# Performance work log

Measured on AMD Instinct MI355X. Metric: run time of the kernel, lower is better.

Reference implementation:

```python
import jax, jax.numpy as jnp
import numpy as np

D_MODEL = 1024
HEADS = 16
D_K = D_MODEL // HEADS
D_FF = 4096
B, S = 4, 2048
EPS = 1e-5


def _layer_norm(x, gamma, beta):
    mu = jnp.mean(x, axis=-1, keepdims=True)
    var = jnp.mean(jnp.square(x - mu), axis=-1, keepdims=True)
    return (x - mu) * jax.lax.rsqrt(var + EPS) * gamma + beta


def setup_inputs() -> dict:
    key = jax.random.key(0)
    ks = jax.random.split(key, 16)
    s_in = 1.0 / np.sqrt(D_MODEL)
    s_ff = 1.0 / np.sqrt(D_FF)
    inp = {
        "x": jax.random.normal(ks[0], (B, S, D_MODEL), dtype=jnp.float32),
        "src_mask": jnp.ones((B, 1, 1, S), dtype=jnp.int32),
        "Wq": jax.random.uniform(ks[1], (D_MODEL, D_MODEL), jnp.float32, -s_in, s_in),
        "bq": jnp.zeros((D_MODEL,), jnp.float32),
        "Wk": jax.random.uniform(ks[2], (D_MODEL, D_MODEL), jnp.float32, -s_in, s_in),
        "bk": jnp.zeros((D_MODEL,), jnp.float32),
        "Wv": jax.random.uniform(ks[3], (D_MODEL, D_MODEL), jnp.float32, -s_in, s_in),
        "bv": jnp.zeros((D_MODEL,), jnp.float32),
        "Wo": jax.random.uniform(ks[4], (D_MODEL, D_MODEL), jnp.float32, -s_in, s_in),
        "bo": jnp.zeros((D_MODEL,), jnp.float32),
        "W1": jax.random.uniform(ks[5], (D_MODEL, D_FF), jnp.float32, -s_in, s_in),
        "b1": jnp.zeros((D_FF,), jnp.float32),
        "W2": jax.random.uniform(ks[6], (D_FF, D_MODEL), jnp.float32, -s_ff, s_ff),
        "b2": jnp.zeros((D_MODEL,), jnp.float32),
        "g1": jnp.ones((D_MODEL,), jnp.float32),
        "be1": jnp.zeros((D_MODEL,), jnp.float32),
        "g2": jnp.ones((D_MODEL,), jnp.float32),
        "be2": jnp.zeros((D_MODEL,), jnp.float32),
    }
    return inp


def reference(x, src_mask, Wq, bq, Wk, bk, Wv, bv, Wo, bo, W1, b1, W2, b2, g1, be1, g2, be2):
    Bn, L, _ = x.shape
    # Self-attention (dropout=0 / eval)
    q = (x @ Wq + bq).reshape(Bn, L, HEADS, D_K).transpose(0, 2, 1, 3)  # [B,H,L,dk]
    k = (x @ Wk + bk).reshape(Bn, L, HEADS, D_K).transpose(0, 2, 1, 3)
    v = (x @ Wv + bv).reshape(Bn, L, HEADS, D_K).transpose(0, 2, 1, 3)
    scores = jnp.einsum("bhqd,bhkd->bhqk", q, k) / np.sqrt(D_K).astype(np.float32)
    scores = jnp.where(src_mask == 0, -jnp.inf, scores)
    attn = jax.nn.softmax(scores, axis=-1)
    out = jnp.einsum("bhqk,bhkd->bhqd", attn, v)
    out = out.transpose(0, 2, 1, 3).reshape(Bn, L, D_MODEL)
    attn_out = out @ Wo + bo
    x = _layer_norm(x + attn_out, g1, be1)
    # FFN
    ffn = jax.nn.relu(x @ W1 + b1) @ W2 + b2
    x = _layer_norm(x + ffn, g2, be2)
    return x
```

## Files before the change

kernel.cpp:

```cpp
#include <hip/hip_runtime.h>
#include <hip/hip_bf16.h>
#include <cstdint>
#include <cstddef>

typedef __bf16 bf16;
typedef __bf16 bf16x8 __attribute__((ext_vector_type(8)));
typedef float  f32x4  __attribute__((ext_vector_type(4)));
typedef unsigned short u16x4 __attribute__((ext_vector_type(4)));
typedef uint32_t u32x4 __attribute__((ext_vector_type(4)));

static constexpr int D_MODEL = 1024;
static constexpr int HEADS   = 16;
static constexpr int D_KH    = 64;
static constexpr int D_FF    = 4096;
static constexpr int BATCH   = 4;
static constexpr int SEQ     = 2048;
static constexpr int MROWS   = BATCH * SEQ;

#define VMCNT(n) asm volatile("s_waitcnt vmcnt(" #n ")" ::: "memory")
#define LGKM0()                                            \
  do {                                                     \
    asm volatile("s_waitcnt lgkmcnt(0)" ::: "memory");     \
    __builtin_amdgcn_sched_barrier(0);                     \
  } while (0)

__device__ __forceinline__ unsigned short bfbits(float f) {
  return __builtin_bit_cast(unsigned short, (bf16)f);
}

__device__ __forceinline__ void gload_lds16(const void* g, void* l) {
  __builtin_amdgcn_global_load_lds(
      (__attribute__((address_space(1))) uint32_t*)(uintptr_t)g,
      (__attribute__((address_space(3))) uint32_t*)(uintptr_t)l, 16, 0, 0);
}

__global__ void k_cast_bf16(const float* __restrict__ in, bf16* __restrict__ out) {
  int i = (blockIdx.x * 256 + threadIdx.x) * 8;
  const float4* p = (const float4*)(in + i);
  float4 a = p[0], b = p[1];
  bf16x8 v;
  v[0] = (bf16)a.x; v[1] = (bf16)a.y; v[2] = (bf16)a.z; v[3] = (bf16)a.w;
  v[4] = (bf16)b.x; v[5] = (bf16)b.y; v[6] = (bf16)b.z; v[7] = (bf16)b.w;
  *(bf16x8*)(out + i) = v;
}

__global__ void k_mask_flags(const int* __restrict__ mask, uint32_t* __restrict__ flags) {
  __shared__ uint32_t sb[4];
  int tid = threadIdx.x;
  if (tid < 4) sb[tid] = 0;
  __syncthreads();
  int b = tid >> 5, t = tid & 31;
  const int4* p = (const int4*)(mask + b * SEQ + t * 64);
  int all = 1;
#pragma unroll
  for (int i = 0; i < 16; ++i) {
    int4 v = p[i];
    all &= v.x & v.y & v.z & v.w;
  }
  if (all) atomicOr(&sb[b], 1u << t);
  __syncthreads();
  if (tid < 4) flags[tid] = sb[tid];
}

struct TP4 { const float* src[4]; bf16* dst[4]; };
__global__ void k_transpose_cast4(TP4 p) {
  __shared__ float tile[64][65];
  const float* W = p.src[blockIdx.z];
  bf16* Wt = p.dst[blockIdx.z];
  int k0 = blockIdx.x * 64, n0 = blockIdx.y * 64;
  int c = threadIdx.x & 63, r0 = threadIdx.x >> 6;
#pragma unroll
  for (int i = 0; i < 16; ++i) {
    int r = r0 + i * 4;
    tile[r][c] = W[(size_t)(k0 + r) * 1024 + n0 + c];
  }
  __syncthreads();
#pragma unroll
  for (int i = 0; i < 16; ++i) {
    int r = r0 + i * 4;
    Wt[(size_t)(n0 + r) * 1024 + k0 + c] = (bf16)tile[c][r];
  }
}

__global__ void k_transpose_cast(const float* __restrict__ W, bf16* __restrict__ Wt,
                                 int K, int N) {
  __shared__ float tile[64][65];
  int k0 = blockIdx.x * 64, n0 = blockIdx.y * 64;
  int c = threadIdx.x & 63, r0 = threadIdx.x >> 6;
#pragma unroll
  for (int i = 0; i < 16; ++i) {
    int r = r0 + i * 4;
    tile[r][c] = W[(size_t)(k0 + r) * N + n0 + c];
  }
  __syncthreads();
#pragma unroll
  for (int i = 0; i < 16; ++i) {
    int r = r0 + i * 4;
    Wt[(size_t)(n0 + r) * K + k0 + c] = (bf16)tile[c][r];
  }
}

enum { EP_RELU = 0, EP_F32 = 1, EP_QKV = 2 };

template <int EPI, int NREP>
__global__ __launch_bounds__(512, 2) void k_gemm8(
    const bf16* __restrict__ A, const bf16* __restrict__ Bt,
    const float* __restrict__ bias, const float* __restrict__ bias2,
    const float* __restrict__ bias3,
    void* __restrict__ Cout, void* __restrict__ C2, void* __restrict__ C3,
    int N, int K) {
  extern __shared__ char smem[];
  constexpr int BN = NREP * 64;
  constexpr int HB = NREP / 2;
  const int tid = threadIdx.x;
  const int lane = tid & 63;
  const int wid = tid >> 6;
  const int wm = wid >> 2, wn = wid & 3;
  const int l15 = lane & 15, l4 = lane >> 4;
  const int bx = blockIdx.x, by = blockIdx.y;
  const int NI = K >> 7;

  const int c0 = tid, c1 = tid + 512;
  const bf16* baseA0 = A + (size_t)(bx * 256 + (c0 >> 3)) * K + ((c0 & 7) ^ ((c0 >> 3) & 7)) * 8;
  const bf16* baseA1 = A + (size_t)(bx * 256 + (c1 >> 3)) * K + ((c1 & 7) ^ ((c1 >> 3) & 7)) * 8;
  const bf16* baseB0 = Bt + (size_t)(by * BN + (c0 >> 3)) * K + ((c0 & 7) ^ ((c0 >> 3) & 7)) * 8;
  const bf16* baseB1 = Bt + (size_t)(by * BN + (c1 >> 3)) * K + ((c1 & 7) ^ ((c1 >> 3) & 7)) * 8;
  const size_t rowK128 = (size_t)128 * K;

  auto stA = [&](int h, int t, int buf) {
    gload_lds16(baseA0 + h * rowK128 + t * 64, smem + buf * 32768 + h * 16384 + c0 * 16);
    gload_lds16(baseA1 + h * rowK128 + t * 64, smem + buf * 32768 + h * 16384 + c1 * 16);
  };
  auto stB = [&](int h, int t, int buf) {
    gload_lds16(baseB0 + h * rowK128 + t * 64,
                smem + 65536 + buf * (HB * 16384) + h * 16384 + c0 * 16);
    gload_lds16(baseB1 + h * rowK128 + t * 64,
                smem + 65536 + buf * (HB * 16384) + h * 16384 + c1 * 16);
  };

  const int ch0 = (l4 ^ (l15 & 7)) * 16;
  const int ch1 = ((4 + l4) ^ (l15 & 7)) * 16;
  const int aoff = l15 * 128;
  int boffh[NREP];
#pragma unroll
  for (int n = 0; n < NREP; ++n) {
    int rB = wn * (NREP * 16) + n * 16 + l15;
    boffh[n] = (rB >> 7) * 16384 + (rB & 127) * 128;
  }

  f32x4 acc[8][NREP] = {};
  bf16x8 breg[NREP][2];

  stA(0, 0, 0); stA(1, 0, 0); stB(0, 0, 0);
  if constexpr (HB == 2) stB(1, 0, 0);
  stA(0, 1, 1); stA(1, 1, 1); stB(0, 1, 1);
  if constexpr (HB == 2) stB(1, 1, 1);

  for (int i = 0; i < NI; ++i) {
    const int t1 = 2 * i + 1, t2 = 2 * i + 2;
    const bool notfirst = (i > 0), notlast = (i + 1 < NI);
#pragma unroll
    for (int p = 0; p < 8; ++p) {
      const int q = p & 3;
      const char* Ab = smem + (p >> 2) * 32768 + wm * 16384;
      const char* Bb = smem + 65536 + (p >> 2) * (HB * 16384);
      if (p == 0) {
        if (notfirst) {
          stA(0, t1, 1);
          VMCNT(2);
        } else {
          if constexpr (HB == 2) VMCNT(8); else VMCNT(6);
        }
        __builtin_amdgcn_s_barrier();
      } else if (p == 4) {
        if (notlast) {
          stA(0, t2, 0);
          VMCNT(2);
        } else {
          VMCNT(0);
        }
        __builtin_amdgcn_s_barrier();
      }
      if (q == 0) {
#pragma unroll
        for (int n = 0; n < NREP; ++n) {
          breg[n][0] = *(const bf16x8*)(Bb + boffh[n] + ch0);
          breg[n][1] = *(const bf16x8*)(Bb + boffh[n] + ch1);
        }
      }
      bf16x8 a0k0 = *(const bf16x8*)(Ab + (2 * q + 0) * 2048 + aoff + ch0);
      bf16x8 a0k1 = *(const bf16x8*)(Ab + (2 * q + 0) * 2048 + aoff + ch1);
      bf16x8 a1k0 = *(const bf16x8*)(Ab + (2 * q + 1) * 2048 + aoff + ch0);
      bf16x8 a1k1 = *(const bf16x8*)(Ab + (2 * q + 1) * 2048 + aoff + ch1);
      if (p == 1) { if (notfirst) stA(1, t1, 1); }
      else if (p == 2) { if (notfirst) stB(0, t1, 1); }
      else if (p == 3) { if constexpr (HB == 2) { if (notfirst) stB(1, t1, 1); } }
      else if (p == 5) { if (notlast) stA(1, t2, 0); }
      else if (p == 6) { if (notlast) stB(0, t2, 0); }
      else if (p == 7) { if constexpr (HB == 2) { if (notlast) stB(1, t2, 0); } }
      if (p != 0 && p != 4) __builtin_amdgcn_s_barrier();
      LGKM0();
      __builtin_amdgcn_s_setprio(1);
#pragma unroll
      for (int n = 0; n < NREP; ++n) {
        acc[2 * q + 0][n] = __builtin_amdgcn_mfma_f32_16x16x32_bf16(a0k0, breg[n][0], acc[2 * q + 0][n], 0, 0, 0);
        acc[2 * q + 0][n] = __builtin_amdgcn_mfma_f32_16x16x32_bf16(a0k1, breg[n][1], acc[2 * q + 0][n], 0, 0, 0);
        acc[2 * q + 1][n] = __builtin_amdgcn_mfma_f32_16x16x32_bf16(a1k0, breg[n][0], acc[2 * q + 1][n], 0, 0, 0);
        acc[2 * q + 1][n] = __builtin_amdgcn_mfma_f32_16x16x32_bf16(a1k1, breg[n][1], acc[2 * q + 1][n], 0, 0, 0);
      }
      __builtin_amdgcn_s_setprio(0);
      __builtin_amdgcn_s_barrier();
    }
  }

  float bia[NREP];
#pragma unroll
  for (int n = 0; n < NREP; ++n) {
    int colL = wn * (NREP * 16) + n * 16 + l15;
    if constexpr (EPI == EP_QKV) {
      const int g = by >> 2;
      const float* bp = (g == 0) ? bias : (g == 1 ? bias2 : bias3);
      bia[n] = bp[(by & 3) * 256 + colL];
    } else {
      bia[n] = bias[by * BN + colL];
    }
  }
#pragma unroll
  for (int mf = 0; mf < 8; ++mf) {
    int row0 = bx * 256 + wm * 128 + mf * 16 + l4 * 4;
#pragma unroll
    for (int n = 0; n < NREP; ++n) {
      int colL = wn * (NREP * 16) + n * 16 + l15;
      if constexpr (EPI == EP_QKV) {
        const int g = by >> 2;
        int cc = (by & 3) * 256 + colL;
        if (g == 2) {
          int bidx = row0 >> 11, s0 = row0 & 2047;
          u16x4 pk;
#pragma unroll
          for (int r = 0; r < 4; ++r) pk[r] = bfbits(acc[mf][n][r] + bia[n]);
          *(u16x4*)((bf16*)C3 + (((size_t)bidx * HEADS + (cc >> 6)) * D_KH + (cc & 63)) * SEQ + s0) = pk;
        } else {
          bf16* dst = g ? (bf16*)C2 : (bf16*)Cout;
#pragma unroll
          for (int r = 0; r < 4; ++r)
            dst[(size_t)(row0 + r) * 1024 + cc] = (bf16)(acc[mf][n][r] + bia[n]);
        }
      } else {
        int col = by * BN + colL;
#pragma unroll
        for (int r = 0; r < 4; ++r) {
          float v = acc[mf][n][r] + bia[n];
          if constexpr (EPI == EP_RELU)
            ((bf16*)Cout)[(size_t)(row0 + r) * N + col] = (bf16)fmaxf(v, 0.f);
          else
            ((float*)Cout)[(size_t)(row0 + r) * N + col] = v;
        }
      }
    }
  }
}

__global__ __launch_bounds__(256, 4) void k_attn(
    const bf16* __restrict__ Q, const bf16* __restrict__ Kb,
    const bf16* __restrict__ Vt, const int* __restrict__ mask,
    const uint32_t* __restrict__ Mf, bf16* __restrict__ O) {
  __shared__ bf16 Ks[2][64 * 64];
  __shared__ bf16 Vs[2][64 * 64];
  const int tid = threadIdx.x;
  const int lane = tid & 63;
  const int l15 = lane & 15, l4 = lane >> 4;
  const int L = blockIdx.x;
  const int xcd = L & 7, rest = L >> 3;
  const int qx = rest & 15, yhi = rest >> 4;
  const int bh = yhi * 8 + xcd;
  const int b = bh >> 4, h = bh & 15;
  const size_t qrow0 = (size_t)b * SEQ + qx * 128 + (tid >> 6) * 32;
  const bf16* Kbase = Kb + (size_t)b * SEQ * D_MODEL + h * 64;
  const bf16* Vbase = Vt + (size_t)bh * D_KH * SEQ;
  const int* mbase = mask + b * SEQ;
  const uint32_t mflags = Mf[b];
  constexpr float C = 0.18033688011f;

  bf16x8 qf[2][2];
#pragma unroll
  for (int m = 0; m < 2; ++m)
#pragma unroll
    for (int ks = 0; ks < 2; ++ks)
      qf[m][ks] = *(const bf16x8*)&Q[(qrow0 + m * 16 + l15) * D_MODEL + h * 64 + ks * 32 + l4 * 8];

  f32x4 o[2][4] = {};
  float lrun[2] = {0.f, 0.f};

  auto stage = [&](int buf, int kv0) {
#pragma unroll
    for (int i = 0; i < 2; ++i) {
      int o_ = tid + i * 256;
      int row = o_ >> 3;
      int ch = (o_ & 7) ^ (row & 7);
      gload_lds16(Kbase + (size_t)(kv0 + row) * D_MODEL + ch * 8,
                  (char*)&Ks[buf][0] + o_ * 16);
      gload_lds16(Vbase + (size_t)row * SEQ + kv0 + ch * 8,
                  (char*)&Vs[buf][0] + o_ * 16);
    }
  };

  stage(0, 0);
  __syncthreads();

  for (int kv0 = 0; kv0 < SEQ; kv0 += 64) {
    const int cur = (kv0 >> 6) & 1;
    if (kv0 + 64 < SEQ) stage(cur ^ 1, kv0 + 64);
    const bf16* Kc = &Ks[cur][0];
    const bf16* Vc = &Vs[cur][0];

    f32x4 sf[2][4] = {};
    __builtin_amdgcn_s_setprio(1);
#pragma unroll
    for (int ks = 0; ks < 2; ++ks)
#pragma unroll
      for (int n = 0; n < 4; ++n) {
        int r = n * 16 + l15;
        bf16x8 kf = *(const bf16x8*)&Kc[r * 64 + ((ks * 32 + l4 * 8) ^ ((r & 7) << 3))];
#pragma unroll
        for (int m = 0; m < 2; ++m)
          sf[m][n] = __builtin_amdgcn_mfma_f32_16x16x32_bf16(kf, qf[m][ks], sf[m][n], 0, 0, 0);
      }
    __builtin_amdgcn_s_setprio(0);

    if (__builtin_expect(!((mflags >> (kv0 >> 6)) & 1), 0)) {
#pragma unroll
      for (int n = 0; n < 4; ++n) {
        int4 mk = *(const int4*)&mbase[kv0 + n * 16 + l4 * 4];
#pragma unroll
        for (int r = 0; r < 4; ++r)
          if (((const int*)&mk)[r] == 0) {
            sf[0][n][r] = -1e30f;
            sf[1][n][r] = -1e30f;
          }
      }
    }

    uint32_t pk[2][4][2];
#pragma unroll
    for (int m = 0; m < 2; ++m) {
      float ps = 0.f;
#pragma unroll
      for (int n = 0; n < 4; ++n) {
#pragma unroll
        for (int r = 0; r < 4; ++r) {
          float pv = exp2f(sf[m][n][r] * C);
          sf[m][n][r] = pv;
          ps += pv;
        }
        asm("v_cvt_pk_bf16_f32 %0, %1, %2"
            : "=v"(pk[m][n][0]) : "v"(sf[m][n][0]), "v"(sf[m][n][1]));
        asm("v_cvt_pk_bf16_f32 %0, %1, %2"
            : "=v"(pk[m][n][1]) : "v"(sf[m][n][2]), "v"(sf[m][n][3]));
      }
      lrun[m] += ps;
    }

    bf16x8 pa[2][2];
#pragma unroll
    for (int m = 0; m < 2; ++m)
#pragma unroll
      for (int ks = 0; ks < 2; ++ks) {
        u32x4 w;
#pragma unroll
        for (int hh = 0; hh < 2; ++hh) {
          uint32_t a = pk[m][ks * 2 + 0][hh];
          uint32_t bsw = pk[m][ks * 2 + 1][hh];
          asm("v_permlane32_swap_b32 %0, %1" : "+v"(a), "+v"(bsw));
          asm("v_permlane16_swap_b32 %0, %1" : "+v"(a), "+v"(bsw));
          w[hh] = a;
          w[2 + hh] = bsw;
        }
        pa[ks][m] = __builtin_bit_cast(bf16x8, w);
      }

#pragma unroll
    for (int ks = 0; ks < 2; ++ks) {
      __builtin_amdgcn_s_setprio(1);
#pragma unroll
      for (int n = 0; n < 4; ++n) {
        int d = n * 16 + l15;
        bf16x8 vf = *(const bf16x8*)&Vc[d * 64 + ((ks * 32 + l4 * 8) ^ ((d & 7) << 3))];
#pragma unroll
        for (int m = 0; m < 2; ++m)
          o[m][n] = __builtin_amdgcn_mfma_f32_16x16x32_bf16(pa[ks][m], vf, o[m][n], 0, 0, 0);
      }
      __builtin_amdgcn_s_setprio(0);
    }
    __syncthreads();
  }

#pragma unroll
  for (int m = 0; m < 2; ++m) {
    lrun[m] += __shfl_xor(lrun[m], 16);
    lrun[m] += __shfl_xor(lrun[m], 32);
  }
#pragma unroll
  for (int m = 0; m < 2; ++m) {
    float inv[4];
#pragma unroll
    for (int r = 0; r < 4; ++r)
      inv[r] = 1.0f / __shfl(lrun[m], l4 * 4 + r);
#pragma unroll
    for (int n = 0; n < 4; ++n)
#pragma unroll
      for (int r = 0; r < 4; ++r)
        O[(qrow0 + m * 16 + l4 * 4 + r) * D_MODEL + h * 64 + n * 16 + l15] =
            (bf16)(o[m][n][r] * inv[r]);
  }
}

__global__ __launch_bounds__(256) void k_add_ln(
    const float* __restrict__ a, const float* __restrict__ b,
    const float* __restrict__ g, const float* __restrict__ be,
    float* __restrict__ yf, bf16* __restrict__ yb) {
  const int t = threadIdx.x;
  const size_t base = (size_t)blockIdx.x * D_MODEL + t * 4;
  float4 va = *(const float4*)(a + base);
  float4 vb = *(const float4*)(b + base);
  float v0 = va.x + vb.x, v1 = va.y + vb.y, v2 = va.z + vb.z, v3 = va.w + vb.w;
  float s  = v0 + v1 + v2 + v3;
  float s2 = v0 * v0 + v1 * v1 + v2 * v2 + v3 * v3;
#pragma unroll
  for (int off = 1; off < 64; off <<= 1) {
    s  += __shfl_xor(s, off);
    s2 += __shfl_xor(s2, off);
  }
  __shared__ float red1[4], red2[4];
  int w = t >> 6;
  if ((t & 63) == 0) { red1[w] = s; red2[w] = s2; }
  __syncthreads();
  s  = red1[0] + red1[1] + red1[2] + red1[3];
  s2 = red2[0] + red2[1] + red2[2] + red2[3];
  float mu  = s * (1.f / D_MODEL);
  float var = s2 * (1.f / D_MODEL) - mu * mu;
  float rstd = rsqrtf(var + 1e-5f);
  float4 vg  = *(const float4*)(g + t * 4);
  float4 vbe = *(const float4*)(be + t * 4);
  float y0 = (v0 - mu) * rstd * vg.x + vbe.x;
  float y1 = (v1 - mu) * rstd * vg.y + vbe.y;
  float y2 = (v2 - mu) * rstd * vg.z + vbe.z;
  float y3 = (v3 - mu) * rstd * vg.w + vbe.w;
  *(float4*)(yf + base) = make_float4(y0, y1, y2, y3);
  if (yb) {
    u16x4 pk = {bfbits(y0), bfbits(y1), bfbits(y2), bfbits(y3)};
    *(u16x4*)(yb + base) = pk;
  }
}

extern "C" void kernel_launch(void* const* d_in, const int* in_sizes, int n_in,
                              void* d_out, int out_size, void* d_ws, size_t ws_size,
                              hipStream_t stream) {
  const float* x   = (const float*)d_in[0];
  const int*  mask = (const int*)d_in[1];
  const float* Wq  = (const float*)d_in[2];
  const float* bq  = (const float*)d_in[3];
  const float* Wk  = (const float*)d_in[4];
  const float* bk_ = (const float*)d_in[5];
  const float* Wv  = (const float*)d_in[6];
  const float* bv  = (const float*)d_in[7];
  const float* Wo  = (const float*)d_in[8];
  const float* bo  = (const float*)d_in[9];
  const float* W1  = (const float*)d_in[10];
  const float* b1  = (const float*)d_in[11];
  const float* W2  = (const float*)d_in[12];
  const float* b2  = (const float*)d_in[13];
  const float* g1  = (const float*)d_in[14];
  const float* be1 = (const float*)d_in[15];
  const float* g2  = (const float*)d_in[16];
  const float* be2 = (const float*)d_in[17];

  char* ws = (char*)d_ws;
  const size_t MB = 1ull << 20;
  bf16*  xb   = (bf16*)(ws + 0);
  bf16*  Qb   = (bf16*)(ws + 16 * MB);
  bf16*  Kbuf = (bf16*)(ws + 32 * MB);
  bf16*  Vt   = (bf16*)(ws + 48 * MB);
  bf16*  Hb   = (bf16*)(ws + 0);
  float* f32a = (float*)(ws + 64 * MB);
  float* x1f  = (float*)(ws + 96 * MB);
  bf16*  x1b  = (bf16*)(ws + 128 * MB);
  bf16*  Wqkvt= (bf16*)(ws + 144 * MB);
  bf16*  Wot  = (bf16*)(ws + 150 * MB);
  bf16*  W1t  = (bf16*)(ws + 152 * MB);
  bf16*  W2t  = (bf16*)(ws + 160 * MB);
  uint32_t* mfl = (uint32_t*)(ws + 64 * MB);
  bf16*  Ob   = xb;

  const int SM4 = 131072, SM2 = 98304;
  hipFuncSetAttribute(reinterpret_cast<const void*>(&k_gemm8<EP_QKV, 4>),
                      hipFuncAttributeMaxDynamicSharedMemorySize, SM4);
  hipFuncSetAttribute(reinterpret_cast<const void*>(&k_gemm8<EP_RELU, 4>),
                      hipFuncAttributeMaxDynamicSharedMemorySize, SM4);
  hipFuncSetAttribute(reinterpret_cast<const void*>(&k_gemm8<EP_F32, 2>),
                      hipFuncAttributeMaxDynamicSharedMemorySize, SM2);

  k_cast_bf16<<<MROWS * D_MODEL / (256 * 8), 256, 0, stream>>>(x, xb);
  k_mask_flags<<<1, 128, 0, stream>>>(mask, mfl);
  TP4 tp;
  tp.src[0] = Wq; tp.dst[0] = Wqkvt;
  tp.src[1] = Wk; tp.dst[1] = Wqkvt + 1024 * 1024;
  tp.src[2] = Wv; tp.dst[2] = Wqkvt + 2 * 1024 * 1024;
  tp.src[3] = Wo; tp.dst[3] = Wot;
  k_transpose_cast4<<<dim3(16, 16, 4), 256, 0, stream>>>(tp);
  k_transpose_cast<<<dim3(16, 64), 256, 0, stream>>>(W1, W1t, 1024, 4096);
  k_transpose_cast<<<dim3(64, 16), 256, 0, stream>>>(W2, W2t, 4096, 1024);

  k_gemm8<EP_QKV, 4><<<dim3(32, 12), 512, SM4, stream>>>(
      xb, Wqkvt, bq, bk_, bv, Qb, Kbuf, Vt, 3072, 1024);

  k_attn<<<1024, 256, 0, stream>>>(Qb, Kbuf, Vt, mask, mfl, Ob);

  k_gemm8<EP_F32, 2><<<dim3(32, 8), 512, SM2, stream>>>(
      Ob, Wot, bo, nullptr, nullptr, f32a, nullptr, nullptr, 1024, 1024);
  k_add_ln<<<MROWS, 256, 0, stream>>>(x, f32a, g1, be1, x1f, x1b);

  k_gemm8<EP_RELU, 4><<<dim3(32, 16), 512, SM4, stream>>>(
      x1b, W1t, b1, nullptr, nullptr, Hb, nullptr, nullptr, 4096, 1024);
  k_gemm8<EP_F32, 2><<<dim3(32, 8), 512, SM2, stream>>>(
      Hb, W2t, b2, nullptr, nullptr, f32a, nullptr, nullptr, 1024, 4096);
  k_add_ln<<<MROWS, 256, 0, stream>>>(x1f, f32a, g2, be2, (float*)d_out, nullptr);
}
```

Measured before the change: 387.4 us.

## Merge prep kernels, fold softmax scale into Q, use bf16 intermediates

Several unrelated changes land together. Mask-flag computation is folded into the x cast kernel, and the weight transpose launches are merged into one. The softmax scale is folded into the Q projection epilogue, and row sums are computed with an extra MFMA against a ones vector instead of scalar adds plus shuffles. The Wo and W2 projection outputs and the residual x1 are stored as bf16 instead of fp32, which cuts memory traffic in the add-layernorm kernels but costs precision in the residual path and the final output.

```diff
diff --git a/kernel.cpp b/kernel.cpp
--- a/kernel.cpp
+++ b/kernel.cpp
@@ -16,6 +16,7 @@
 static constexpr int BATCH   = 4;
 static constexpr int SEQ     = 2048;
 static constexpr int MROWS   = BATCH * SEQ;
+static constexpr float QSCALE = 0.18033688011f;
 
 #define VMCNT(n) asm volatile("s_waitcnt vmcnt(" #n ")" ::: "memory")
 #define LGKM0()                                            \
@@ -27,6 +28,9 @@
 __device__ __forceinline__ unsigned short bfbits(float f) {
   return __builtin_bit_cast(unsigned short, (bf16)f);
 }
+__device__ __forceinline__ float bf2f(unsigned short u) {
+  return __builtin_bit_cast(float, (uint32_t)u << 16);
+}
 
 __device__ __forceinline__ void gload_lds16(const void* g, void* l) {
   __builtin_amdgcn_global_load_lds(
@@ -34,7 +38,28 @@
       (__attribute__((address_space(3))) uint32_t*)(uintptr_t)l, 16, 0, 0);
 }
 
-__global__ void k_cast_bf16(const float* __restrict__ in, bf16* __restrict__ out) {
+__global__ void k_cast_mask(const float* __restrict__ in, bf16* __restrict__ out,
+                            const int* __restrict__ mask, uint32_t* __restrict__ flags) {
+  if (blockIdx.x == 4096) {
+    __shared__ uint32_t sb[4];
+    int tid = threadIdx.x;
+    if (tid < 4) sb[tid] = 0;
+    __syncthreads();
+    if (tid < 128) {
+      int b = tid >> 5, t = tid & 31;
+      const int4* p = (const int4*)(mask + b * SEQ + t * 64);
+      int all = 1;
+#pragma unroll
+      for (int i = 0; i < 16; ++i) {
+        int4 v = p[i];
+        all &= v.x & v.y & v.z & v.w;
+      }
+      if (all) atomicOr(&sb[b], 1u << t);
+    }
+    __syncthreads();
+    if (tid < 4) flags[tid] = sb[tid];
+    return;
+  }
   int i = (blockIdx.x * 256 + threadIdx.x) * 8;
   const float4* p = (const float4*)(in + i);
   float4 a = p[0], b = p[1];
@@ -44,48 +69,29 @@
   *(bf16x8*)(out + i) = v;
 }
 
-__global__ void k_mask_flags(const int* __restrict__ mask, uint32_t* __restrict__ flags) {
-  __shared__ uint32_t sb[4];
-  int tid = threadIdx.x;
-  if (tid < 4) sb[tid] = 0;
-  __syncthreads();
-  int b = tid >> 5, t = tid & 31;
-  const int4* p = (const int4*)(mask + b * SEQ + t * 64);
-  int all = 1;
-#pragma unroll
-  for (int i = 0; i < 16; ++i) {
-    int4 v = p[i];
-    all &= v.x & v.y & v.z & v.w;
-  }
-  if (all) atomicOr(&sb[b], 1u << t);
-  __syncthreads();
-  if (tid < 4) flags[tid] = sb[tid];
-}
-
-struct TP4 { const float* src[4]; bf16* dst[4]; };
-__global__ void k_transpose_cast4(TP4 p) {
+struct TPAll {
+  const float* w1; const float* w2; const float* wx[4];
+  bf16* w1t; bf16* w2t; bf16* wxt[4];
+};
+__global__ void k_transpose_all(TPAll p) {
   __shared__ float tile[64][65];
-  const float* W = p.src[blockIdx.z];
-  bf16* Wt = p.dst[blockIdx.z];
-  int k0 = blockIdx.x * 64, n0 = blockIdx.y * 64;
-  int c = threadIdx.x & 63, r0 = threadIdx.x >> 6;
-#pragma unroll
-  for (int i = 0; i < 16; ++i) {
-    int r = r0 + i * 4;
-    tile[r][c] = W[(size_t)(k0 + r) * 1024 + n0 + c];
-  }
-  __syncthreads();
-#pragma unroll
-  for (int i = 0; i < 16; ++i) {
-    int r = r0 + i * 4;
-    Wt[(size_t)(n0 + r) * 1024 + k0 + c] = (bf16)tile[c][r];
-  }
-}
-
-__global__ void k_transpose_cast(const float* __restrict__ W, bf16* __restrict__ Wt,
-                                 int K, int N) {
-  __shared__ float tile[64][65];
-  int k0 = blockIdx.x * 64, n0 = blockIdx.y * 64;
+  const float* W;
+  bf16* Wt;
+  int K, N, k0, n0;
+  int t = blockIdx.x;
+  if (t < 1024) {
+    W = p.w1; Wt = p.w1t; K = 1024; N = 4096;
+    k0 = (t & 15) * 64; n0 = (t >> 4) * 64;
+  } else if (t < 2048) {
+    int u = t - 1024;
+    W = p.w2; Wt = p.w2t; K = 4096; N = 1024;
+    k0 = (u & 63) * 64; n0 = (u >> 6) * 64;
+  } else {
+    int u = t - 2048;
+    int which = u >> 8, v = u & 255;
+    W = p.wx[which]; Wt = p.wxt[which]; K = 1024; N = 1024;
+    k0 = (v & 15) * 64; n0 = (v >> 4) * 64;
+  }
   int c = threadIdx.x & 63, r0 = threadIdx.x >> 6;
 #pragma unroll
   for (int i = 0; i < 16; ++i) {
@@ -100,7 +106,7 @@
   }
 }
 
-enum { EP_RELU = 0, EP_F32 = 1, EP_QKV = 2 };
+enum { EP_RELU = 0, EP_O16 = 1, EP_QKV = 2 };
 
 template <int EPI, int NREP>
 __global__ __launch_bounds__(512, 2) void k_gemm8(
@@ -240,8 +246,13 @@
 #pragma unroll
           for (int r = 0; r < 4; ++r) pk[r] = bfbits(acc[mf][n][r] + bia[n]);
           *(u16x4*)((bf16*)C3 + (((size_t)bidx * HEADS + (cc >> 6)) * D_KH + (cc & 63)) * SEQ + s0) = pk;
+        } else if (g == 0) {
+          bf16* dst = (bf16*)Cout;
+#pragma unroll
+          for (int r = 0; r < 4; ++r)
+            dst[(size_t)(row0 + r) * 1024 + cc] = (bf16)((acc[mf][n][r] + bia[n]) * QSCALE);
         } else {
-          bf16* dst = g ? (bf16*)C2 : (bf16*)Cout;
+          bf16* dst = (bf16*)C2;
 #pragma unroll
           for (int r = 0; r < 4; ++r)
             dst[(size_t)(row0 + r) * 1024 + cc] = (bf16)(acc[mf][n][r] + bia[n]);
@@ -251,10 +262,8 @@
 #pragma unroll
         for (int r = 0; r < 4; ++r) {
           float v = acc[mf][n][r] + bia[n];
-          if constexpr (EPI == EP_RELU)
-            ((bf16*)Cout)[(size_t)(row0 + r) * N + col] = (bf16)fmaxf(v, 0.f);
-          else
-            ((float*)Cout)[(size_t)(row0 + r) * N + col] = v;
+          if constexpr (EPI == EP_RELU) v = fmaxf(v, 0.f);
+          ((bf16*)Cout)[(size_t)(row0 + r) * N + col] = (bf16)v;
         }
       }
     }
@@ -280,7 +289,6 @@
   const bf16* Vbase = Vt + (size_t)bh * D_KH * SEQ;
   const int* mbase = mask + b * SEQ;
   const uint32_t mflags = Mf[b];
-  constexpr float C = 0.18033688011f;
 
   bf16x8 qf[2][2];
 #pragma unroll
@@ -290,7 +298,10 @@
       qf[m][ks] = *(const bf16x8*)&Q[(qrow0 + m * 16 + l15) * D_MODEL + h * 64 + ks * 32 + l4 * 8];
 
   f32x4 o[2][4] = {};
-  float lrun[2] = {0.f, 0.f};
+  f32x4 rs[2] = {};
+  bf16x8 ones;
+#pragma unroll
+  for (int i = 0; i < 8; ++i) ones[i] = (bf16)1.0f;
 
   auto stage = [&](int buf, int kv0) {
 #pragma unroll
@@ -344,21 +355,15 @@
     uint32_t pk[2][4][2];
 #pragma unroll
     for (int m = 0; m < 2; ++m) {
-      float ps = 0.f;
 #pragma unroll
       for (int n = 0; n < 4; ++n) {
 #pragma unroll
-        for (int r = 0; r < 4; ++r) {
-          float pv = exp2f(sf[m][n][r] * C);
-          sf[m][n][r] = pv;
-          ps += pv;
-        }
+        for (int r = 0; r < 4; ++r) sf[m][n][r] = exp2f(sf[m][n][r]);
         asm("v_cvt_pk_bf16_f32 %0, %1, %2"
             : "=v"(pk[m][n][0]) : "v"(sf[m][n][0]), "v"(sf[m][n][1]));
         asm("v_cvt_pk_bf16_f32 %0, %1, %2"
             : "=v"(pk[m][n][1]) : "v"(sf[m][n][2]), "v"(sf[m][n][3]));
       }
-      lrun[m] += ps;
     }
 
     bf16x8 pa[2][2];
@@ -390,22 +395,19 @@
         for (int m = 0; m < 2; ++m)
           o[m][n] = __builtin_amdgcn_mfma_f32_16x16x32_bf16(pa[ks][m], vf, o[m][n], 0, 0, 0);
       }
+#pragma unroll
+      for (int m = 0; m < 2; ++m)
+        rs[m] = __builtin_amdgcn_mfma_f32_16x16x32_bf16(pa[ks][m], ones, rs[m], 0, 0, 0);
       __builtin_amdgcn_s_setprio(0);
     }
     __syncthreads();
   }
 
-#pragma unroll
-  for (int m = 0; m < 2; ++m) {
-    lrun[m] += __shfl_xor(lrun[m], 16);
-    lrun[m] += __shfl_xor(lrun[m], 32);
-  }
 #pragma unroll
   for (int m = 0; m < 2; ++m) {
     float inv[4];
 #pragma unroll
-    for (int r = 0; r < 4; ++r)
-      inv[r] = 1.0f / __shfl(lrun[m], l4 * 4 + r);
+    for (int r = 0; r < 4; ++r) inv[r] = 1.0f / rs[m][r];
 #pragma unroll
     for (int n = 0; n < 4; ++n)
 #pragma unroll
@@ -415,15 +417,16 @@
   }
 }
 
-__global__ __launch_bounds__(256) void k_add_ln(
-    const float* __restrict__ a, const float* __restrict__ b,
+__global__ __launch_bounds__(256) void k_add_ln1(
+    const float* __restrict__ a, const bf16* __restrict__ b,
     const float* __restrict__ g, const float* __restrict__ be,
-    float* __restrict__ yf, bf16* __restrict__ yb) {
+    bf16* __restrict__ y) {
   const int t = threadIdx.x;
   const size_t base = (size_t)blockIdx.x * D_MODEL + t * 4;
   float4 va = *(const float4*)(a + base);
-  float4 vb = *(const float4*)(b + base);
-  float v0 = va.x + vb.x, v1 = va.y + vb.y, v2 = va.z + vb.z, v3 = va.w + vb.w;
+  u16x4 vb = *(const u16x4*)(b + base);
+  float v0 = va.x + bf2f(vb[0]), v1 = va.y + bf2f(vb[1]);
+  float v2 = va.z + bf2f(vb[2]), v3 = va.w + bf2f(vb[3]);
   float s  = v0 + v1 + v2 + v3;
   float s2 = v0 * v0 + v1 * v1 + v2 * v2 + v3 * v3;
 #pragma unroll
@@ -442,15 +445,45 @@
   float rstd = rsqrtf(var + 1e-5f);
   float4 vg  = *(const float4*)(g + t * 4);
   float4 vbe = *(const float4*)(be + t * 4);
-  float y0 = (v0 - mu) * rstd * vg.x + vbe.x;
-  float y1 = (v1 - mu) * rstd * vg.y + vbe.y;
-  float y2 = (v2 - mu) * rstd * vg.z + vbe.z;
-  float y3 = (v3 - mu) * rstd * vg.w + vbe.w;
-  *(float4*)(yf + base) = make_float4(y0, y1, y2, y3);
-  if (yb) {
-    u16x4 pk = {bfbits(y0), bfbits(y1), bfbits(y2), bfbits(y3)};
-    *(u16x4*)(yb + base) = pk;
-  }
+  u16x4 pk = {bfbits((v0 - mu) * rstd * vg.x + vbe.x),
+              bfbits((v1 - mu) * rstd * vg.y + vbe.y),
+              bfbits((v2 - mu) * rstd * vg.z + vbe.z),
+              bfbits((v3 - mu) * rstd * vg.w + vbe.w)};
+  *(u16x4*)(y + base) = pk;
+}
+
+__global__ __launch_bounds__(256) void k_add_ln2(
+    const bf16* __restrict__ a, const bf16* __restrict__ b,
+    const float* __restrict__ g, const float* __restrict__ be,
+    float* __restrict__ y) {
+  const int t = threadIdx.x;
+  const size_t base = (size_t)blockIdx.x * D_MODEL + t * 4;
+  u16x4 va = *(const u16x4*)(a + base);
+  u16x4 vb = *(const u16x4*)(b + base);
+  float v0 = bf2f(va[0]) + bf2f(vb[0]), v1 = bf2f(va[1]) + bf2f(vb[1]);
+  float v2 = bf2f(va[2]) + bf2f(vb[2]), v3 = bf2f(va[3]) + bf2f(vb[3]);
+  float s  = v0 + v1 + v2 + v3;
+  float s2 = v0 * v0 + v1 * v1 + v2 * v2 + v3 * v3;
+#pragma unroll
+  for (int off = 1; off < 64; off <<= 1) {
+    s  += __shfl_xor(s, off);
+    s2 += __shfl_xor(s2, off);
+  }
+  __shared__ float red1[4], red2[4];
+  int w = t >> 6;
+  if ((t & 63) == 0) { red1[w] = s; red2[w] = s2; }
+  __syncthreads();
+  s  = red1[0] + red1[1] + red1[2] + red1[3];
+  s2 = red2[0] + red2[1] + red2[2] + red2[3];
+  float mu  = s * (1.f / D_MODEL);
+  float var = s2 * (1.f / D_MODEL) - mu * mu;
+  float rstd = rsqrtf(var + 1e-5f);
+  float4 vg  = *(const float4*)(g + t * 4);
+  float4 vbe = *(const float4*)(be + t * 4);
+  *(float4*)(y + base) = make_float4((v0 - mu) * rstd * vg.x + vbe.x,
+                                     (v1 - mu) * rstd * vg.y + vbe.y,
+                                     (v2 - mu) * rstd * vg.z + vbe.z,
+                                     (v3 - mu) * rstd * vg.w + vbe.w);
 }
 
 extern "C" void kernel_launch(void* const* d_in, const int* in_sizes, int n_in,
@@ -477,52 +510,51 @@
 
   char* ws = (char*)d_ws;
   const size_t MB = 1ull << 20;
-  bf16*  xb   = (bf16*)(ws + 0);
-  bf16*  Qb   = (bf16*)(ws + 16 * MB);
-  bf16*  Kbuf = (bf16*)(ws + 32 * MB);
-  bf16*  Vt   = (bf16*)(ws + 48 * MB);
-  bf16*  Hb   = (bf16*)(ws + 0);
-  float* f32a = (float*)(ws + 64 * MB);
-  float* x1f  = (float*)(ws + 96 * MB);
-  bf16*  x1b  = (bf16*)(ws + 128 * MB);
-  bf16*  Wqkvt= (bf16*)(ws + 144 * MB);
-  bf16*  Wot  = (bf16*)(ws + 150 * MB);
-  bf16*  W1t  = (bf16*)(ws + 152 * MB);
-  bf16*  W2t  = (bf16*)(ws + 160 * MB);
-  uint32_t* mfl = (uint32_t*)(ws + 64 * MB);
-  bf16*  Ob   = xb;
+  bf16*  xb    = (bf16*)(ws + 0);
+  bf16*  Qb    = (bf16*)(ws + 16 * MB);
+  bf16*  Kbuf  = (bf16*)(ws + 32 * MB);
+  bf16*  Vt    = (bf16*)(ws + 48 * MB);
+  bf16*  Hb    = (bf16*)(ws + 0);
+  bf16*  aproj = (bf16*)(ws + 64 * MB);
+  bf16*  f2o   = (bf16*)(ws + 80 * MB);
+  uint32_t* mfl = (uint32_t*)(ws + 96 * MB);
+  bf16*  x1b   = (bf16*)(ws + 128 * MB);
+  bf16*  Wqkvt = (bf16*)(ws + 144 * MB);
+  bf16*  Wot   = (bf16*)(ws + 150 * MB);
+  bf16*  W1t   = (bf16*)(ws + 152 * MB);
+  bf16*  W2t   = (bf16*)(ws + 160 * MB);
+  bf16*  Ob    = xb;
 
   const int SM4 = 131072, SM2 = 98304;
   hipFuncSetAttribute(reinterpret_cast<const void*>(&k_gemm8<EP_QKV, 4>),
                       hipFuncAttributeMaxDynamicSharedMemorySize, SM4);
   hipFuncSetAttribute(reinterpret_cast<const void*>(&k_gemm8<EP_RELU, 4>),
                       hipFuncAttributeMaxDynamicSharedMemorySize, SM4);
-  hipFuncSetAttribute(reinterpret_cast<const void*>(&k_gemm8<EP_F32, 2>),
+  hipFuncSetAttribute(reinterpret_cast<const void*>(&k_gemm8<EP_O16, 2>),
                       hipFuncAttributeMaxDynamicSharedMemorySize, SM2);
 
-  k_cast_bf16<<<MROWS * D_MODEL / (256 * 8), 256, 0, stream>>>(x, xb);
-  k_mask_flags<<<1, 128, 0, stream>>>(mask, mfl);
-  TP4 tp;
-  tp.src[0] = Wq; tp.dst[0] = Wqkvt;
-  tp.src[1] = Wk; tp.dst[1] = Wqkvt + 1024 * 1024;
-  tp.src[2] = Wv; tp.dst[2] = Wqkvt + 2 * 1024 * 1024;
-  tp.src[3] = Wo; tp.dst[3] = Wot;
-  k_transpose_cast4<<<dim3(16, 16, 4), 256, 0, stream>>>(tp);
-  k_transpose_cast<<<dim3(16, 64), 256, 0, stream>>>(W1, W1t, 1024, 4096);
-  k_transpose_cast<<<dim3(64, 16), 256, 0, stream>>>(W2, W2t, 4096, 1024);
+  k_cast_mask<<<4097, 256, 0, stream>>>(x, xb, mask, mfl);
+  TPAll tp;
+  tp.w1 = W1; tp.w1t = W1t;
+  tp.w2 = W2; tp.w2t = W2t;
+  tp.wx[0] = Wq; tp.wxt[0] = Wqkvt;
+  tp.wx[1] = Wk; tp.wxt[1] = Wqkvt + 1024 * 1024;
+  tp.wx[2] = Wv; tp.wxt[2] = Wqkvt + 2 * 1024 * 1024;
+  tp.wx[3] = Wo; tp.wxt[3] = Wot;
+  k_transpose_all<<<3072, 256, 0, stream>>>(tp);
 
   k_gemm8<EP_QKV, 4><<<dim3(32, 12), 512, SM4, stream>>>(
       xb, Wqkvt, bq, bk_, bv, Qb, Kbuf, Vt, 3072, 1024);
 
   k_attn<<<1024, 256, 0, stream>>>(Qb, Kbuf, Vt, mask, mfl, Ob);
 
-  k_gemm8<EP_F32, 2><<<dim3(32, 8), 512, SM2, stream>>>(
-      Ob, Wot, bo, nullptr, nullptr, f32a, nullptr, nullptr, 1024, 1024);
-  k_add_ln<<<MROWS, 256, 0, stream>>>(x, f32a, g1, be1, x1f, x1b);
+  k_gemm8<EP_O16, 2><<<dim3(32, 8), 512, SM2, stream>>>(
+      Ob, Wot, bo, nullptr, nullptr, aproj, nullptr, nullptr, 1024, 1024);
+  k_add_ln1<<<MROWS, 256, 0, stream>>>(x, aproj, g1, be1, x1b);
 
   k_gemm8<EP_RELU, 4><<<dim3(32, 16), 512, SM4, stream>>>(
       x1b, W1t, b1, nullptr, nullptr, Hb, nullptr, nullptr, 4096, 1024);
-  k_gemm8<EP_F32, 2><<<dim3(32, 8), 512, SM2, stream>>>(
-      Hb, W2t, b2, nullptr, nullptr, f32a, nullptr, nullptr, 1024, 4096);
-  k_add_ln<<<MROWS, 256, 0, stream>>>(x1f, f32a, g2, be2, (float*)d_out, nullptr);
-}
+  k_gemm8<EP_O16, 2><<<dim3(32, 8), 512, SM2, stream>>>(
+      Hb, W2t, b2, nullptr, nullptr, f2o, nullptr, nullptr, 1024, 4096);
+  k_add_ln2<<<MROWS, 256, 0, stream>>>(x1b, f2o, g2, be2, (float*)d_out);
+}
```

Measured after the change: 359.4 us. 7.2% less time.
